# Kernel optimization log

Hardware: AMD Instinct MI355X
Metric: run time of the kernel (lower is better)

Reference implementation:

```python
import jax, jax.numpy as jnp
import numpy as np

N, E, H, L = 20000, 1_280_000, 64, 4


def setup_inputs() -> dict:
    key = jax.random.key(0)
    ks = jax.random.split(key, 24)
    inputs = jax.random.normal(ks[0], (1, N, 6), jnp.float32)
    node_masks = jnp.ones((1, N), jnp.int32)
    send_edges = jax.random.randint(ks[1], (E,), 0, N)
    recv_edges = jax.random.randint(ks[2], (E,), 0, N)

    def w(k, shape, scale=None):
        s = (1.0 / np.sqrt(shape[-2])) if scale is None else scale
        return (jax.random.normal(k, shape, jnp.float32) * s)

    d = dict(
        inputs=inputs, node_masks=node_masks,
        send_edges=send_edges, recv_edges=recv_edges,
        emb_w=w(ks[3], (1, H)), emb_b=jnp.zeros((H,), jnp.float32),
        edge_w1=w(ks[4], (L, 2 * H + 1, H)), edge_b1=jnp.zeros((L, H), jnp.float32),
        edge_w2=w(ks[5], (L, H, H)), edge_b2=jnp.zeros((L, H), jnp.float32),
        node_w1=w(ks[6], (L, 2 * H, H)), node_b1=jnp.zeros((L, H), jnp.float32),
        node_w2=w(ks[7], (L, H, H)), node_b2=jnp.zeros((L, H), jnp.float32),
        coord_w1=w(ks[8], (L, H, H)), coord_b1=jnp.zeros((L, H), jnp.float32),
        coord_wout=w(ks[9], (L, H, 1), scale=0.001),  # xavier gain=0.001, no bias
        vel_w1=w(ks[10], (L, H, H)), vel_b1=jnp.zeros((L, H), jnp.float32),
        vel_w2=w(ks[11], (L, H, 1)), vel_b2=jnp.zeros((L, 1), jnp.float32),
    )
    return d


def reference(inputs, node_masks, send_edges, recv_edges,
              emb_w, emb_b, edge_w1, edge_b1, edge_w2, edge_b2,
              node_w1, node_b1, node_w2, node_b2,
              coord_w1, coord_b1, coord_wout,
              vel_w1, vel_b1, vel_w2, vel_b2):
    silu = jax.nn.silu
    # node_masks is all-ones -> node_inds = arange(N); all nodes active.
    pos, vel = jnp.split(inputs, 2, axis=-1)          # [1,N,3] each
    h = jnp.linalg.norm(vel, axis=-1, keepdims=True)  # speed -> [1,N,1]
    h = h @ emb_w + emb_b                             # [1,N,H]
    coord = pos
    n = coord.shape[1]
    counts = jax.ops.segment_sum(jnp.ones_like(recv_edges, dtype=coord.dtype),
                                 recv_edges, num_segments=n)
    inv_cnt = (1.0 / jnp.maximum(counts, 1.0))[None, :, None]
    seg = lambda e: jax.ops.segment_sum(e, recv_edges, num_segments=n)

    for l in range(L):
        # coord2radial
        cd = coord[:, send_edges] - coord[:, recv_edges]        # [1,E,3]
        radial = jnp.sum(cd * cd, -1, keepdims=True)            # [1,E,1]
        # edge_model
        ef_in = jnp.concatenate([h[:, send_edges], h[:, recv_edges], radial], -1)
        ef = silu(silu(ef_in @ edge_w1[l] + edge_b1[l]) @ edge_w2[l] + edge_b2[l])
        # coord_model
        cm = silu(ef @ coord_w1[l] + coord_b1[l]) @ coord_wout[l]  # [1,E,1]
        trans = jnp.clip(cd * cm, -100.0, 100.0)
        agg_mean = jax.vmap(seg)(trans) * inv_cnt                  # scatter_mean
        # velocity update
        v_gate = silu(h @ vel_w1[l] + vel_b1[l]) @ vel_w2[l] + vel_b2[l]
        vel = agg_mean + v_gate * vel
        coord = coord + vel
        # node_model (recurrent residual)
        agg_sum = jax.vmap(seg)(ef)                                # scatter_sum
        hn = jnp.concatenate([h, agg_sum], -1)
        h = silu(hn @ node_w1[l] + node_b1[l]) @ node_w2[l] + node_b2[l] + h

    pred = jnp.concatenate([coord, vel], -1)  # [1,N,6] == pred_all (all active)
    return pred
```

## Files before the change

### kernel.cpp

```cpp
#include <hip/hip_runtime.h>
#include <math.h>

#define N_NODES 20000
#define N_EDGES 1280000
#define NLAYERS 4
#define NTILE (N_EDGES/32)
#define TSTRIDE 68

typedef short bf16x8 __attribute__((ext_vector_type(8)));
typedef float f32x4  __attribute__((ext_vector_type(4)));
typedef long long i64;
typedef unsigned short us;

__device__ __forceinline__ float silu_f(float x) {
    return x / (1.0f + __expf(-x));
}

__device__ __forceinline__ us f2b(float x) {
    union { float f; unsigned u; } v; v.f = x;
    unsigned r = v.u + 0x7FFF + ((v.u >> 16) & 1);
    return (us)(r >> 16);
}
__device__ __forceinline__ float b2f(us u) {
    union { float f; unsigned u; } v; v.u = ((unsigned)u) << 16;
    return v.f;
}
__device__ __forceinline__ void split2r(float x, us& hi, us& lo) {
    hi = f2b(x);
    lo = f2b(x - b2f(hi));
}
__device__ __forceinline__ void split2f(float x, us& hi, us& lo) {
    union { float f; unsigned u; } v; v.f = x;
    hi = (us)(v.u >> 16);
    union { float f; unsigned u; } h; h.u = v.u & 0xFFFF0000u;
    union { float f; unsigned u; } r; r.f = x - h.f;
    lo = (us)(r.u >> 16);
}

__device__ __forceinline__ bf16x8 ld8(const us* p) {
    bf16x8 a;
    ((i64*)&a)[0] = *(const i64*)p;
    ((i64*)&a)[1] = *(const i64*)(p + 4);
    return a;
}

__device__ __forceinline__ void mfma3(f32x4& acc, bf16x8 ahi, bf16x8 alo,
                                      bf16x8 bhi, bf16x8 blo) {
    acc = __builtin_amdgcn_mfma_f32_16x16x32_bf16(ahi, bhi, acc, 0, 0, 0);
    acc = __builtin_amdgcn_mfma_f32_16x16x32_bf16(alo, bhi, acc, 0, 0, 0);
    acc = __builtin_amdgcn_mfma_f32_16x16x32_bf16(ahi, blo, acc, 0, 0, 0);
}

__global__ void k_init(const float* __restrict__ inp,
                       const float* __restrict__ emb_w,
                       const float* __restrict__ emb_b,
                       float* __restrict__ outv,
                       us* __restrict__ hbh, us* __restrict__ hbl) {
    int t = blockIdx.x * blockDim.x + threadIdx.x;
    int n = t >> 6, f = t & 63;
    if (n >= N_NODES) return;
    float vx = inp[n*6+3], vy = inp[n*6+4], vz = inp[n*6+5];
    float sp = sqrtf(vx*vx + vy*vy + vz*vz);
    float hv = sp * emb_w[f] + emb_b[f];
    us hi, lo; split2r(hv, hi, lo);
    hbh[t] = hi; hbl[t] = lo;
    if (f < 6) outv[n*6+f] = inp[n*6+f];
}

__global__ void k_cnt(const int* __restrict__ recv, int* __restrict__ counts) {
    int t = blockIdx.x*256 + threadIdx.x;
    if (t < N_EDGES) atomicAdd(&counts[recv[t]], 1);
}

__global__ void k_scan(const int* __restrict__ counts, int* __restrict__ rowstart,
                       int* __restrict__ cursor) {
    __shared__ int buf[256];
    __shared__ int carry;
    const int tid = threadIdx.x;
    if (tid == 0) carry = 0;
    __syncthreads();
    for (int base = 0; base < N_NODES; base += 256) {
        const int i = base + tid;
        int v = (i < N_NODES) ? counts[i] : 0;
        buf[tid] = v;
        __syncthreads();
        for (int off = 1; off < 256; off <<= 1) {
            int tv = (tid >= off) ? buf[tid-off] : 0;
            __syncthreads();
            buf[tid] += tv;
            __syncthreads();
        }
        const int excl = buf[tid] - v;
        if (i < N_NODES) { int rv = carry + excl; rowstart[i] = rv; cursor[i] = rv; }
        __syncthreads();
        if (tid == 255) carry += buf[255];
        __syncthreads();
    }
    if (tid < 20) rowstart[N_NODES + tid] = N_EDGES;
}

__global__ void k_scatter(const int* __restrict__ send, const int* __restrict__ recv,
                          int* __restrict__ cursor, us* __restrict__ sp16) {
    int t = blockIdx.x*256 + threadIdx.x;
    if (t < N_EDGES) {
        int p = atomicAdd(&cursor[recv[t]], 1);
        sp16[p] = (us)send[t];
    }
}

__global__ void k_tilemap(const int* __restrict__ rowstart, int* __restrict__ tile2node) {
    int b = blockIdx.x*256 + threadIdx.x;
    if (b >= NTILE) return;
    const int e = b*32;
    int lo = 0, hi = N_NODES-1;
    while (lo < hi) {
        int mid = (lo+hi+1) >> 1;
        if (rowstart[mid] <= e) lo = mid; else hi = mid-1;
    }
    tile2node[b] = lo;
}

__global__ void k_prepw(const float* __restrict__ ew1, const float* __restrict__ ew2,
                        const float* __restrict__ cw1,
                        us* __restrict__ w1th, us* __restrict__ w1tl,
                        us* __restrict__ w2th, us* __restrict__ w2tl,
                        us* __restrict__ cw1th, us* __restrict__ cw1tl) {
    int t = blockIdx.x*256 + threadIdx.x;
    int l = t >> 14;
    int r = t & 16383;
    us hi, lo;
    if (r < 8192) {
        int n = r >> 7, k = r & 127;
        split2r(ew1[l*129*64 + k*64 + n], hi, lo);
        w1th[l*8192 + r] = hi; w1tl[l*8192 + r] = lo;
    } else if (r < 12288) {
        int rr = r - 8192; int n = rr >> 6, k = rr & 63;
        split2r(ew2[l*4096 + k*64 + n], hi, lo);
        w2th[l*4096 + n*64 + k] = hi; w2tl[l*4096 + n*64 + k] = lo;
    } else {
        int rr = r - 12288; int n = rr >> 6, k = rr & 63;
        split2r(cw1[l*4096 + k*64 + n], hi, lo);
        cw1th[l*4096 + n*64 + k] = hi; cw1tl[l*4096 + n*64 + k] = lo;
    }
}

__launch_bounds__(256, 4)
__global__ void k_edge(const us* __restrict__ sp16, const int* __restrict__ rowstart,
                       const int* __restrict__ tile2node,
                       const us* __restrict__ hbh, const us* __restrict__ hbl,
                       const float* __restrict__ outv,
                       const us* __restrict__ w1th, const us* __restrict__ w1tl,
                       const us* __restrict__ w2th, const us* __restrict__ w2tl,
                       const us* __restrict__ cw1th, const us* __restrict__ cw1tl,
                       const float* __restrict__ ew1, const float* __restrict__ eb1,
                       const float* __restrict__ eb2, const float* __restrict__ cb1,
                       const float* __restrict__ cwo,
                       float* __restrict__ aggs, float* __restrict__ aggm) {
    __shared__ us tileh[4][32*TSTRIDE];
    __shared__ us tilel[4][32*TSTRIDE];

    const int tid  = threadIdx.x;
    const int wid  = tid >> 6;
    const int lane = tid & 63;
    const int q    = lane >> 4;
    const int l15  = lane & 15;
    const int wbase = blockIdx.x*128 + wid*32;
    const int wtile = blockIdx.x*4 + wid;

    const int e0 = wbase + l15, e1 = e0 + 16;
    const int s0 = sp16[e0], s1 = sp16[e1];

    const int t2n = tile2node[wtile];
    const int wv = rowstart[t2n + 1 + l15];
    int seg0 = 0, seg1 = 0;
    #pragma unroll
    for (int i = 0; i < 16; ++i) {
        const int wi = __shfl(wv, i);
        seg0 += (e0 >= wi);
        seg1 += (e1 >= wi);
    }
    const int r0 = t2n + seg0, r1 = t2n + seg1;

    const float cdx0 = outv[s0*6+0]-outv[r0*6+0], cdy0 = outv[s0*6+1]-outv[r0*6+1], cdz0 = outv[s0*6+2]-outv[r0*6+2];
    const float cdx1 = outv[s1*6+0]-outv[r1*6+0], cdy1 = outv[s1*6+1]-outv[r1*6+1], cdz1 = outv[s1*6+2]-outv[r1*6+2];
    const float rad0 = cdx0*cdx0+cdy0*cdy0+cdz0*cdz0;
    const float rad1 = cdx1*cdx1+cdy1*cdy1+cdz1*cdz1;

    f32x4 acc[2][4];
    #pragma unroll
    for (int mu = 0; mu < 2; ++mu)
        #pragma unroll
        for (int t = 0; t < 4; ++t) acc[mu][t] = (f32x4){0.f,0.f,0.f,0.f};

    #pragma unroll
    for (int kc = 0; kc < 4; ++kc) {
        const int off = (kc & 1)*32 + q*8;
        const size_t o0 = (size_t)((kc < 2) ? s0 : r0)*64 + off;
        const size_t o1 = (size_t)((kc < 2) ? s1 : r1)*64 + off;
        bf16x8 a0h = ld8(hbh + o0), a0l = ld8(hbl + o0);
        bf16x8 a1h = ld8(hbh + o1), a1l = ld8(hbl + o1);
        #pragma unroll
        for (int t = 0; t < 4; ++t) {
            const int wo = (16*t + l15)*128 + kc*32 + q*8;
            bf16x8 bh = ld8(w1th + wo), bl = ld8(w1tl + wo);
            mfma3(acc[0][t], a0h, a0l, bh, bl);
            mfma3(acc[1][t], a1h, a1l, bh, bl);
        }
    }

    float rsh0[4], rsh1[4];
    #pragma unroll
    for (int r = 0; r < 4; ++r) {
        rsh0[r] = __shfl(rad0, 4*q + r);
        rsh1[r] = __shfl(rad1, 4*q + r);
    }
    #pragma unroll
    for (int t = 0; t < 4; ++t) {
        const int col = 16*t + l15;
        const float wl = ew1[128*64 + col];
        const float bb = eb1[col];
        #pragma unroll
        for (int r = 0; r < 4; ++r) {
            acc[0][t][r] += rsh0[r]*wl + bb;
            acc[1][t][r] += rsh1[r]*wl + bb;
        }
    }

    us* Th = tileh[wid];
    us* Tl = tilel[wid];
    #pragma unroll
    for (int mu = 0; mu < 2; ++mu)
        #pragma unroll
        for (int t = 0; t < 4; ++t)
            #pragma unroll
            for (int r = 0; r < 4; ++r) {
                us hi, lo; split2f(silu_f(acc[mu][t][r]), hi, lo);
                const int ti = (mu*16 + 4*q + r)*TSTRIDE + 16*t + l15;
                Th[ti] = hi; Tl[ti] = lo;
            }
    __asm__ volatile("s_waitcnt lgkmcnt(0)" ::: "memory");

    #pragma unroll
    for (int mu = 0; mu < 2; ++mu)
        #pragma unroll
        for (int t = 0; t < 4; ++t) acc[mu][t] = (f32x4){0.f,0.f,0.f,0.f};
    #pragma unroll
    for (int kc = 0; kc < 2; ++kc) {
        const int t0 = l15*TSTRIDE + kc*32 + q*8;
        const int t1i = (16+l15)*TSTRIDE + kc*32 + q*8;
        bf16x8 a0h = ld8(Th + t0),  a0l = ld8(Tl + t0);
        bf16x8 a1h = ld8(Th + t1i), a1l = ld8(Tl + t1i);
        #pragma unroll
        for (int t = 0; t < 4; ++t) {
            const int wo = (16*t + l15)*64 + kc*32 + q*8;
            bf16x8 bh = ld8(w2th + wo), bl = ld8(w2tl + wo);
            mfma3(acc[0][t], a0h, a0l, bh, bl);
            mfma3(acc[1][t], a1h, a1l, bh, bl);
        }
    }

    float ef[2][4][4];
    #pragma unroll
    for (int t = 0; t < 4; ++t) {
        const float bb = eb2[16*t + l15];
        #pragma unroll
        for (int mu = 0; mu < 2; ++mu)
            #pragma unroll
            for (int r = 0; r < 4; ++r)
                ef[mu][t][r] = silu_f(acc[mu][t][r] + bb);
    }
    __asm__ volatile("s_waitcnt lgkmcnt(0)" ::: "memory");
    #pragma unroll
    for (int mu = 0; mu < 2; ++mu)
        #pragma unroll
        for (int t = 0; t < 4; ++t)
            #pragma unroll
            for (int r = 0; r < 4; ++r) {
                us hi, lo; split2f(ef[mu][t][r], hi, lo);
                const int ti = (mu*16 + 4*q + r)*TSTRIDE + 16*t + l15;
                Th[ti] = hi; Tl[ti] = lo;
            }
    __asm__ volatile("s_waitcnt lgkmcnt(0)" ::: "memory");

    #pragma unroll
    for (int mu = 0; mu < 2; ++mu)
        #pragma unroll
        for (int t = 0; t < 4; ++t) acc[mu][t] = (f32x4){0.f,0.f,0.f,0.f};
    #pragma unroll
    for (int kc = 0; kc < 2; ++kc) {
        const int t0 = l15*TSTRIDE + kc*32 + q*8;
        const int t1i = (16+l15)*TSTRIDE + kc*32 + q*8;
        bf16x8 a0h = ld8(Th + t0),  a0l = ld8(Tl + t0);
        bf16x8 a1h = ld8(Th + t1i), a1l = ld8(Tl + t1i);
        #pragma unroll
        for (int t = 0; t < 4; ++t) {
            const int wo = (16*t + l15)*64 + kc*32 + q*8;
            bf16x8 bh = ld8(cw1th + wo), bl = ld8(cw1tl + wo);
            mfma3(acc[0][t], a0h, a0l, bh, bl);
            mfma3(acc[1][t], a1h, a1l, bh, bl);
        }
    }

    float cm0[4] = {0.f,0.f,0.f,0.f}, cm1[4] = {0.f,0.f,0.f,0.f};
    #pragma unroll
    for (int t = 0; t < 4; ++t) {
        const int col = 16*t + l15;
        const float cb = cb1[col];
        const float co = cwo[col];
        #pragma unroll
        for (int r = 0; r < 4; ++r) {
            cm0[r] += silu_f(acc[0][t][r] + cb) * co;
            cm1[r] += silu_f(acc[1][t][r] + cb) * co;
        }
    }
    #pragma unroll
    for (int m = 1; m <= 8; m <<= 1)
        #pragma unroll
        for (int r = 0; r < 4; ++r) {
            cm0[r] += __shfl_xor(cm0[r], m);
            cm1[r] += __shfl_xor(cm1[r], m);
        }

    int   sgrow[2][4];
    float tv[2][4];
    #pragma unroll
    for (int mu = 0; mu < 2; ++mu)
        #pragma unroll
        for (int r = 0; r < 4; ++r) {
            sgrow[mu][r] = __shfl(mu ? seg1 : seg0, 4*q + r);
            const float cxv = __shfl(mu ? cdx1 : cdx0, 4*q + r);
            const float cyv = __shfl(mu ? cdy1 : cdy0, 4*q + r);
            const float czv = __shfl(mu ? cdz1 : cdz0, 4*q + r);
            const float cmv = mu ? cm1[r] : cm0[r];
            const float sel = (l15 == 0) ? cxv : (l15 == 1) ? cyv : czv;
            tv[mu][r] = (l15 < 3) ? fminf(fmaxf(sel*cmv, -100.f), 100.f) : 0.f;
        }

    const int segA = __shfl(seg0, 0);
    const int segB = __shfl(seg1, 15);

    if (segB == segA) {
        float s4[4], trT = 0.f;
        #pragma unroll
        for (int t = 0; t < 4; ++t) {
            float v = 0.f;
            #pragma unroll
            for (int mu = 0; mu < 2; ++mu)
                #pragma unroll
                for (int r = 0; r < 4; ++r) v += ef[mu][t][r];
            v += __shfl_xor(v, 16);
            v += __shfl_xor(v, 32);
            s4[t] = v;
        }
        #pragma unroll
        for (int mu = 0; mu < 2; ++mu)
            #pragma unroll
            for (int r = 0; r < 4; ++r) trT += tv[mu][r];
        trT += __shfl_xor(trT, 16);
        trT += __shfl_xor(trT, 32);
        const int rn = t2n + segA;
        if (q == 0) {
            #pragma unroll
            for (int t = 0; t < 4; ++t)
                atomicAdd(&aggs[(size_t)rn*64 + 16*t + l15], s4[t]);
            if (l15 < 3) atomicAdd(&aggm[rn*3 + l15], trT);
        }
    } else if (segB == segA + 1) {
        float sA[4] = {0,0,0,0}, sB[4] = {0,0,0,0};
        float trA = 0.f, trB = 0.f;
        #pragma unroll
        for (int mu = 0; mu < 2; ++mu)
            #pragma unroll
            for (int r = 0; r < 4; ++r) {
                const bool isA = (sgrow[mu][r] == segA);
                #pragma unroll
                for (int t = 0; t < 4; ++t) {
                    const float v = ef[mu][t][r];
                    sA[t] += isA ? v : 0.f;
                    sB[t] += isA ? 0.f : v;
                }
                const float tvv = tv[mu][r];
                trA += isA ? tvv : 0.f;
                trB += isA ? 0.f : tvv;
            }
        #pragma unroll
        for (int t = 0; t < 4; ++t) {
            sA[t] += __shfl_xor(sA[t], 16); sA[t] += __shfl_xor(sA[t], 32);
            sB[t] += __shfl_xor(sB[t], 16); sB[t] += __shfl_xor(sB[t], 32);
        }
        trA += __shfl_xor(trA, 16); trA += __shfl_xor(trA, 32);
        trB += __shfl_xor(trB, 16); trB += __shfl_xor(trB, 32);
        const int rnA = t2n + segA, rnB = rnA + 1;
        if (q == 0) {
            #pragma unroll
            for (int t = 0; t < 4; ++t) {
                atomicAdd(&aggs[(size_t)rnA*64 + 16*t + l15], sA[t]);
                atomicAdd(&aggs[(size_t)rnB*64 + 16*t + l15], sB[t]);
            }
            if (l15 < 3) {
                atomicAdd(&aggm[rnA*3 + l15], trA);
                atomicAdd(&aggm[rnB*3 + l15], trB);
            }
        }
    } else {
        #pragma unroll
        for (int mu = 0; mu < 2; ++mu)
            #pragma unroll
            for (int r = 0; r < 4; ++r) {
                const int ren = t2n + sgrow[mu][r];
                #pragma unroll
                for (int t = 0; t < 4; ++t)
                    atomicAdd(&aggs[(size_t)ren*64 + 16*t + l15], ef[mu][t][r]);
                if (l15 < 3) atomicAdd(&aggm[ren*3 + l15], tv[mu][r]);
            }
    }
}

__launch_bounds__(256, 4)
__global__ void k_node(const float* __restrict__ aggs, const float* __restrict__ aggm,
                       const int* __restrict__ rowstart,
                       const float* __restrict__ VW1, const float* __restrict__ vb1,
                       const float* __restrict__ VW2, const float* __restrict__ vb2,
                       const float* __restrict__ NW1, const float* __restrict__ nb1,
                       const float* __restrict__ NW2, const float* __restrict__ nb2,
                       float* __restrict__ outv,
                       us* __restrict__ hbh, us* __restrict__ hbl) {
    __shared__ float hs[4][64], as[4][64], tt[4][64];
    const int tid = threadIdx.x;
    const int nn = tid >> 6, f = tid & 63;
    const int n = blockIdx.x*4 + nn;
    float hv = b2f(hbh[n*64+f]) + b2f(hbl[n*64+f]);
    hs[nn][f] = hv;
    as[nn][f] = aggs[n*64+f];
    __syncthreads();

    float a1 = vb1[f];
    for (int k = 0; k < 64; ++k) a1 += hs[nn][k] * VW1[k*64+f];
    float p = silu_f(a1) * VW2[f];
    #pragma unroll
    for (int o = 32; o > 0; o >>= 1) p += __shfl_down(p, o);
    float vgate = __shfl(p, 0) + vb2[0];

    if (f < 3) {
        float icnt = 1.0f / fmaxf((float)(rowstart[n+1] - rowstart[n]), 1.0f);
        float nv = aggm[n*3+f]*icnt + vgate*outv[n*6+3+f];
        outv[n*6+3+f] = nv;
        outv[n*6+f]  += nv;
    }

    float b = nb1[f];
    for (int k = 0; k < 64; ++k) b += hs[nn][k]*NW1[k*64+f];
    for (int k = 0; k < 64; ++k) b += as[nn][k]*NW1[(64+k)*64+f];
    __syncthreads();
    tt[nn][f] = silu_f(b);
    __syncthreads();
    float o = nb2[f] + hv;
    for (int k = 0; k < 64; ++k) o += tt[nn][k]*NW2[k*64+f];
    us hi, lo; split2r(o, hi, lo);
    hbh[n*64+f] = hi; hbl[n*64+f] = lo;
}

extern "C" void kernel_launch(void* const* d_in, const int* in_sizes, int n_in,
                              void* d_out, int out_size, void* d_ws, size_t ws_size,
                              hipStream_t stream) {
    const float* inp   = (const float*)d_in[0];
    const int*   send  = (const int*)d_in[2];
    const int*   recv  = (const int*)d_in[3];
    const float* emb_w = (const float*)d_in[4];
    const float* emb_b = (const float*)d_in[5];
    const float* ew1   = (const float*)d_in[6];
    const float* eb1   = (const float*)d_in[7];
    const float* ew2   = (const float*)d_in[8];
    const float* eb2   = (const float*)d_in[9];
    const float* nw1   = (const float*)d_in[10];
    const float* nb1   = (const float*)d_in[11];
    const float* nw2   = (const float*)d_in[12];
    const float* nb2   = (const float*)d_in[13];
    const float* cw1   = (const float*)d_in[14];
    const float* cb1   = (const float*)d_in[15];
    const float* cwo   = (const float*)d_in[16];
    const float* vw1   = (const float*)d_in[17];
    const float* vb1   = (const float*)d_in[18];
    const float* vw2   = (const float*)d_in[19];
    const float* vb2   = (const float*)d_in[20];

    float* outv = (float*)d_out;

    float* ws        = (float*)d_ws;
    float* aggs      = ws;
    float* aggm      = aggs + (size_t)N_NODES*64;
    int*   rowstart  = (int*)(aggm + N_NODES*3);
    int*   tile2node = rowstart + (N_NODES+20);
    us*    hbh       = (us*)(tile2node + NTILE);
    us*    hbl       = hbh + (size_t)N_NODES*64;
    us*    sp16      = hbl + (size_t)N_NODES*64;
    us*    w1th      = sp16 + N_EDGES;
    us*    w1tl      = w1th + 4*8192;
    us*    w2th      = w1tl + 4*8192;
    us*    w2tl      = w2th + 4*4096;
    us*    cw1th     = w2tl + 4*4096;
    us*    cw1tl     = cw1th + 4*4096;
    int*   counts    = (int*)aggs;
    int*   cursor    = counts + N_NODES;

    hipMemsetAsync(counts, 0, N_NODES*sizeof(int), stream);
    k_init<<<(N_NODES*64)/256, 256, 0, stream>>>(inp, emb_w, emb_b, outv, hbh, hbl);
    k_cnt<<<(N_EDGES+255)/256, 256, 0, stream>>>(recv, counts);
    k_scan<<<1, 256, 0, stream>>>(counts, rowstart, cursor);
    k_scatter<<<(N_EDGES+255)/256, 256, 0, stream>>>(send, recv, cursor, sp16);
    k_tilemap<<<(NTILE+255)/256, 256, 0, stream>>>(rowstart, tile2node);
    k_prepw<<<256, 256, 0, stream>>>(ew1, ew2, cw1, w1th, w1tl, w2th, w2tl, cw1th, cw1tl);

    for (int l = 0; l < NLAYERS; ++l) {
        hipMemsetAsync(aggs, 0, (size_t)N_NODES*67*sizeof(float), stream);
        k_edge<<<N_EDGES/128, 256, 0, stream>>>(sp16, rowstart, tile2node, hbh, hbl, outv,
            w1th + l*8192, w1tl + l*8192,
            w2th + l*4096, w2tl + l*4096,
            cw1th + l*4096, cw1tl + l*4096,
            ew1 + (size_t)l*129*64, eb1 + l*64, eb2 + l*64,
            cb1 + l*64, cwo + l*64,
            aggs, aggm);
        k_node<<<N_NODES/4, 256, 0, stream>>>(aggs, aggm, rowstart,
            vw1 + (size_t)l*64*64, vb1 + l*64, vw2 + l*64, vb2 + l,
            nw1 + (size_t)l*128*64, nb1 + l*64,
            nw2 + (size_t)l*64*64,  nb2 + l*64,
            outv, hbh, hbl);
    }
}
```

Baseline: 2.082 ms.

## Process edge halves sequentially for occupancy, fuse tilemap into scan, drop memsets

The edge kernel now runs its three-GEMM MLP chain on each 16-edge half in turn instead of both halves together. This halves the LDS tile and accumulator registers, so launch bounds rise from 4 to 6 waves per SIMD. The tile-to-node map is built inside a chunked single-block scan, removing the binary-search kernel. The per-layer memset of the aggregation buffers is replaced by zeroing them in the node kernel after they are read. The cost is less instruction-level parallelism per wave and a more serial scan.

```diff
diff --git a/kernel.cpp b/kernel.cpp
--- a/kernel.cpp
+++ b/kernel.cpp
@@ -6,6 +6,7 @@
 #define NLAYERS 4
 #define NTILE (N_EDGES/32)
 #define TSTRIDE 68
+#define SCHUNK 79
 
 typedef short bf16x8 __attribute__((ext_vector_type(8)));
 typedef float f32x4  __attribute__((ext_vector_type(4)));
@@ -73,28 +74,27 @@
 }
 
 __global__ void k_scan(const int* __restrict__ counts, int* __restrict__ rowstart,
-                       int* __restrict__ cursor) {
+                       int* __restrict__ cursor, int* __restrict__ tile2node) {
     __shared__ int buf[256];
-    __shared__ int carry;
     const int tid = threadIdx.x;
-    if (tid == 0) carry = 0;
+    const int lo = tid*SCHUNK;
+    const int hi = (lo + SCHUNK < N_NODES) ? lo + SCHUNK : N_NODES;
+    int s = 0;
+    for (int i = lo; i < hi; ++i) s += counts[i];
+    buf[tid] = s;
     __syncthreads();
-    for (int base = 0; base < N_NODES; base += 256) {
-        const int i = base + tid;
-        int v = (i < N_NODES) ? counts[i] : 0;
-        buf[tid] = v;
+    for (int off = 1; off < 256; off <<= 1) {
+        int v = (tid >= off) ? buf[tid-off] : 0;
         __syncthreads();
-        for (int off = 1; off < 256; off <<= 1) {
-            int tv = (tid >= off) ? buf[tid-off] : 0;
-            __syncthreads();
-            buf[tid] += tv;
-            __syncthreads();
-        }
-        const int excl = buf[tid] - v;
-        if (i < N_NODES) { int rv = carry + excl; rowstart[i] = rv; cursor[i] = rv; }
+        buf[tid] += v;
         __syncthreads();
-        if (tid == 255) carry += buf[255];
-        __syncthreads();
+    }
+    int run = buf[tid] - s;
+    for (int i = lo; i < hi; ++i) {
+        rowstart[i] = run; cursor[i] = run;
+        const int c = counts[i];
+        for (int t = (run + 31) >> 5; t*32 < run + c; ++t) tile2node[t] = i;
+        run += c;
     }
     if (tid < 20) rowstart[N_NODES + tid] = N_EDGES;
 }
@@ -106,18 +106,6 @@
         int p = atomicAdd(&cursor[recv[t]], 1);
         sp16[p] = (us)send[t];
     }
-}
-
-__global__ void k_tilemap(const int* __restrict__ rowstart, int* __restrict__ tile2node) {
-    int b = blockIdx.x*256 + threadIdx.x;
-    if (b >= NTILE) return;
-    const int e = b*32;
-    int lo = 0, hi = N_NODES-1;
-    while (lo < hi) {
-        int mid = (lo+hi+1) >> 1;
-        if (rowstart[mid] <= e) lo = mid; else hi = mid-1;
-    }
-    tile2node[b] = lo;
 }
 
 __global__ void k_prepw(const float* __restrict__ ew1, const float* __restrict__ ew2,
@@ -144,7 +132,7 @@
     }
 }
 
-__launch_bounds__(256, 4)
+__launch_bounds__(256, 6)
 __global__ void k_edge(const us* __restrict__ sp16, const int* __restrict__ rowstart,
                        const int* __restrict__ tile2node,
                        const us* __restrict__ hbh, const us* __restrict__ hbl,
@@ -156,8 +144,8 @@
                        const float* __restrict__ eb2, const float* __restrict__ cb1,
                        const float* __restrict__ cwo,
                        float* __restrict__ aggs, float* __restrict__ aggm) {
-    __shared__ us tileh[4][32*TSTRIDE];
-    __shared__ us tilel[4][32*TSTRIDE];
+    __shared__ us tileh[4][16*TSTRIDE];
+    __shared__ us tilel[4][16*TSTRIDE];
 
     const int tid  = threadIdx.x;
     const int wid  = tid >> 6;
@@ -186,140 +174,126 @@
     const float rad0 = cdx0*cdx0+cdy0*cdy0+cdz0*cdz0;
     const float rad1 = cdx1*cdx1+cdy1*cdy1+cdz1*cdz1;
 
-    f32x4 acc[2][4];
-    #pragma unroll
-    for (int mu = 0; mu < 2; ++mu)
-        #pragma unroll
-        for (int t = 0; t < 4; ++t) acc[mu][t] = (f32x4){0.f,0.f,0.f,0.f};
-
-    #pragma unroll
-    for (int kc = 0; kc < 4; ++kc) {
-        const int off = (kc & 1)*32 + q*8;
-        const size_t o0 = (size_t)((kc < 2) ? s0 : r0)*64 + off;
-        const size_t o1 = (size_t)((kc < 2) ? s1 : r1)*64 + off;
-        bf16x8 a0h = ld8(hbh + o0), a0l = ld8(hbl + o0);
-        bf16x8 a1h = ld8(hbh + o1), a1l = ld8(hbl + o1);
-        #pragma unroll
-        for (int t = 0; t < 4; ++t) {
-            const int wo = (16*t + l15)*128 + kc*32 + q*8;
-            bf16x8 bh = ld8(w1th + wo), bl = ld8(w1tl + wo);
-            mfma3(acc[0][t], a0h, a0l, bh, bl);
-            mfma3(acc[1][t], a1h, a1l, bh, bl);
-        }
-    }
-
-    float rsh0[4], rsh1[4];
-    #pragma unroll
-    for (int r = 0; r < 4; ++r) {
-        rsh0[r] = __shfl(rad0, 4*q + r);
-        rsh1[r] = __shfl(rad1, 4*q + r);
-    }
+    float wlv[4], b1v[4], eb2v[4], cb1v[4], cwov[4];
     #pragma unroll
     for (int t = 0; t < 4; ++t) {
         const int col = 16*t + l15;
-        const float wl = ew1[128*64 + col];
-        const float bb = eb1[col];
-        #pragma unroll
-        for (int r = 0; r < 4; ++r) {
-            acc[0][t][r] += rsh0[r]*wl + bb;
-            acc[1][t][r] += rsh1[r]*wl + bb;
-        }
+        wlv[t]  = ew1[128*64 + col];
+        b1v[t]  = eb1[col];
+        eb2v[t] = eb2[col];
+        cb1v[t] = cb1[col];
+        cwov[t] = cwo[col];
     }
 
     us* Th = tileh[wid];
     us* Tl = tilel[wid];
+
+    float ef[2][4][4];
+    float cm[2][4];
+
     #pragma unroll
-    for (int mu = 0; mu < 2; ++mu)
+    for (int mu = 0; mu < 2; ++mu) {
+        const int   sE   = mu ? s1 : s0;
+        const int   rE   = mu ? r1 : r0;
+        const float radE = mu ? rad1 : rad0;
+
+        f32x4 acc[4];
+        #pragma unroll
+        for (int t = 0; t < 4; ++t) acc[t] = (f32x4){0.f,0.f,0.f,0.f};
+        #pragma unroll
+        for (int kc = 0; kc < 4; ++kc) {
+            const int off = (kc & 1)*32 + q*8;
+            const size_t oA = (size_t)((kc < 2) ? sE : rE)*64 + off;
+            bf16x8 ah = ld8(hbh + oA), al = ld8(hbl + oA);
+            #pragma unroll
+            for (int t = 0; t < 4; ++t) {
+                const int wo = (16*t + l15)*128 + kc*32 + q*8;
+                bf16x8 bh = ld8(w1th + wo), bl = ld8(w1tl + wo);
+                mfma3(acc[t], ah, al, bh, bl);
+            }
+        }
+
+        float rsh[4];
+        #pragma unroll
+        for (int r = 0; r < 4; ++r) rsh[r] = __shfl(radE, 4*q + r);
         #pragma unroll
         for (int t = 0; t < 4; ++t)
             #pragma unroll
+            for (int r = 0; r < 4; ++r)
+                acc[t][r] += rsh[r]*wlv[t] + b1v[t];
+
+        #pragma unroll
+        for (int t = 0; t < 4; ++t)
+            #pragma unroll
             for (int r = 0; r < 4; ++r) {
-                us hi, lo; split2f(silu_f(acc[mu][t][r]), hi, lo);
-                const int ti = (mu*16 + 4*q + r)*TSTRIDE + 16*t + l15;
+                us hi, lo; split2f(silu_f(acc[t][r]), hi, lo);
+                const int ti = (4*q + r)*TSTRIDE + 16*t + l15;
                 Th[ti] = hi; Tl[ti] = lo;
             }
-    __asm__ volatile("s_waitcnt lgkmcnt(0)" ::: "memory");
-
-    #pragma unroll
-    for (int mu = 0; mu < 2; ++mu)
-        #pragma unroll
-        for (int t = 0; t < 4; ++t) acc[mu][t] = (f32x4){0.f,0.f,0.f,0.f};
-    #pragma unroll
-    for (int kc = 0; kc < 2; ++kc) {
-        const int t0 = l15*TSTRIDE + kc*32 + q*8;
-        const int t1i = (16+l15)*TSTRIDE + kc*32 + q*8;
-        bf16x8 a0h = ld8(Th + t0),  a0l = ld8(Tl + t0);
-        bf16x8 a1h = ld8(Th + t1i), a1l = ld8(Tl + t1i);
-        #pragma unroll
-        for (int t = 0; t < 4; ++t) {
-            const int wo = (16*t + l15)*64 + kc*32 + q*8;
-            bf16x8 bh = ld8(w2th + wo), bl = ld8(w2tl + wo);
-            mfma3(acc[0][t], a0h, a0l, bh, bl);
-            mfma3(acc[1][t], a1h, a1l, bh, bl);
-        }
-    }
-
-    float ef[2][4][4];
-    #pragma unroll
-    for (int t = 0; t < 4; ++t) {
-        const float bb = eb2[16*t + l15];
-        #pragma unroll
-        for (int mu = 0; mu < 2; ++mu)
+        __asm__ volatile("s_waitcnt lgkmcnt(0)" ::: "memory");
+
+        f32x4 acc2[4];
+        #pragma unroll
+        for (int t = 0; t < 4; ++t) acc2[t] = (f32x4){0.f,0.f,0.f,0.f};
+        #pragma unroll
+        for (int kc = 0; kc < 2; ++kc) {
+            const int to = l15*TSTRIDE + kc*32 + q*8;
+            bf16x8 ah = ld8(Th + to), al = ld8(Tl + to);
+            #pragma unroll
+            for (int t = 0; t < 4; ++t) {
+                const int wo = (16*t + l15)*64 + kc*32 + q*8;
+                bf16x8 bh = ld8(w2th + wo), bl = ld8(w2tl + wo);
+                mfma3(acc2[t], ah, al, bh, bl);
+            }
+        }
+
+        #pragma unroll
+        for (int t = 0; t < 4; ++t)
             #pragma unroll
             for (int r = 0; r < 4; ++r)
-                ef[mu][t][r] = silu_f(acc[mu][t][r] + bb);
-    }
-    __asm__ volatile("s_waitcnt lgkmcnt(0)" ::: "memory");
-    #pragma unroll
-    for (int mu = 0; mu < 2; ++mu)
+                ef[mu][t][r] = silu_f(acc2[t][r] + eb2v[t]);
+        __asm__ volatile("s_waitcnt lgkmcnt(0)" ::: "memory");
         #pragma unroll
         for (int t = 0; t < 4; ++t)
             #pragma unroll
             for (int r = 0; r < 4; ++r) {
                 us hi, lo; split2f(ef[mu][t][r], hi, lo);
-                const int ti = (mu*16 + 4*q + r)*TSTRIDE + 16*t + l15;
+                const int ti = (4*q + r)*TSTRIDE + 16*t + l15;
                 Th[ti] = hi; Tl[ti] = lo;
             }
-    __asm__ volatile("s_waitcnt lgkmcnt(0)" ::: "memory");
-
-    #pragma unroll
-    for (int mu = 0; mu < 2; ++mu)
-        #pragma unroll
-        for (int t = 0; t < 4; ++t) acc[mu][t] = (f32x4){0.f,0.f,0.f,0.f};
-    #pragma unroll
-    for (int kc = 0; kc < 2; ++kc) {
-        const int t0 = l15*TSTRIDE + kc*32 + q*8;
-        const int t1i = (16+l15)*TSTRIDE + kc*32 + q*8;
-        bf16x8 a0h = ld8(Th + t0),  a0l = ld8(Tl + t0);
-        bf16x8 a1h = ld8(Th + t1i), a1l = ld8(Tl + t1i);
-        #pragma unroll
-        for (int t = 0; t < 4; ++t) {
-            const int wo = (16*t + l15)*64 + kc*32 + q*8;
-            bf16x8 bh = ld8(cw1th + wo), bl = ld8(cw1tl + wo);
-            mfma3(acc[0][t], a0h, a0l, bh, bl);
-            mfma3(acc[1][t], a1h, a1l, bh, bl);
-        }
-    }
-
-    float cm0[4] = {0.f,0.f,0.f,0.f}, cm1[4] = {0.f,0.f,0.f,0.f};
-    #pragma unroll
-    for (int t = 0; t < 4; ++t) {
-        const int col = 16*t + l15;
-        const float cb = cb1[col];
-        const float co = cwo[col];
-        #pragma unroll
-        for (int r = 0; r < 4; ++r) {
-            cm0[r] += silu_f(acc[0][t][r] + cb) * co;
-            cm1[r] += silu_f(acc[1][t][r] + cb) * co;
-        }
-    }
-    #pragma unroll
-    for (int m = 1; m <= 8; m <<= 1)
-        #pragma unroll
-        for (int r = 0; r < 4; ++r) {
-            cm0[r] += __shfl_xor(cm0[r], m);
-            cm1[r] += __shfl_xor(cm1[r], m);
-        }
+        __asm__ volatile("s_waitcnt lgkmcnt(0)" ::: "memory");
+
+        f32x4 acc3[4];
+        #pragma unroll
+        for (int t = 0; t < 4; ++t) acc3[t] = (f32x4){0.f,0.f,0.f,0.f};
+        #pragma unroll
+        for (int kc = 0; kc < 2; ++kc) {
+            const int to = l15*TSTRIDE + kc*32 + q*8;
+            bf16x8 ah = ld8(Th + to), al = ld8(Tl + to);
+            #pragma unroll
+            for (int t = 0; t < 4; ++t) {
+                const int wo = (16*t + l15)*64 + kc*32 + q*8;
+                bf16x8 bh = ld8(cw1th + wo), bl = ld8(cw1tl + wo);
+                mfma3(acc3[t], ah, al, bh, bl);
+            }
+        }
+
+        float cmE[4] = {0.f,0.f,0.f,0.f};
+        #pragma unroll
+        for (int t = 0; t < 4; ++t)
+            #pragma unroll
+            for (int r = 0; r < 4; ++r)
+                cmE[r] += silu_f(acc3[t][r] + cb1v[t]) * cwov[t];
+        #pragma unroll
+        for (int m = 1; m <= 8; m <<= 1)
+            #pragma unroll
+            for (int r = 0; r < 4; ++r)
+                cmE[r] += __shfl_xor(cmE[r], m);
+        #pragma unroll
+        for (int r = 0; r < 4; ++r) cm[mu][r] = cmE[r];
+
+        __asm__ volatile("s_waitcnt lgkmcnt(0)" ::: "memory");
+    }
 
     int   sgrow[2][4];
     float tv[2][4];
@@ -331,7 +305,7 @@
             const float cxv = __shfl(mu ? cdx1 : cdx0, 4*q + r);
             const float cyv = __shfl(mu ? cdy1 : cdy0, 4*q + r);
             const float czv = __shfl(mu ? cdz1 : cdz0, 4*q + r);
-            const float cmv = mu ? cm1[r] : cm0[r];
+            const float cmv = cm[mu][r];
             const float sel = (l15 == 0) ? cxv : (l15 == 1) ? cyv : czv;
             tv[mu][r] = (l15 < 3) ? fminf(fmaxf(sel*cmv, -100.f), 100.f) : 0.f;
         }
@@ -417,7 +391,7 @@
 }
 
 __launch_bounds__(256, 4)
-__global__ void k_node(const float* __restrict__ aggs, const float* __restrict__ aggm,
+__global__ void k_node(float* __restrict__ aggs, float* __restrict__ aggm,
                        const int* __restrict__ rowstart,
                        const float* __restrict__ VW1, const float* __restrict__ vb1,
                        const float* __restrict__ VW2, const float* __restrict__ vb2,
@@ -432,6 +406,7 @@
     float hv = b2f(hbh[n*64+f]) + b2f(hbl[n*64+f]);
     hs[nn][f] = hv;
     as[nn][f] = aggs[n*64+f];
+    aggs[n*64+f] = 0.f;
     __syncthreads();
 
     float a1 = vb1[f];
@@ -444,6 +419,7 @@
     if (f < 3) {
         float icnt = 1.0f / fmaxf((float)(rowstart[n+1] - rowstart[n]), 1.0f);
         float nv = aggm[n*3+f]*icnt + vgate*outv[n*6+3+f];
+        aggm[n*3+f] = 0.f;
         outv[n*6+3+f] = nv;
         outv[n*6+f]  += nv;
     }
@@ -506,13 +482,12 @@
     hipMemsetAsync(counts, 0, N_NODES*sizeof(int), stream);
     k_init<<<(N_NODES*64)/256, 256, 0, stream>>>(inp, emb_w, emb_b, outv, hbh, hbl);
     k_cnt<<<(N_EDGES+255)/256, 256, 0, stream>>>(recv, counts);
-    k_scan<<<1, 256, 0, stream>>>(counts, rowstart, cursor);
+    k_scan<<<1, 256, 0, stream>>>(counts, rowstart, cursor, tile2node);
     k_scatter<<<(N_EDGES+255)/256, 256, 0, stream>>>(send, recv, cursor, sp16);
-    k_tilemap<<<(NTILE+255)/256, 256, 0, stream>>>(rowstart, tile2node);
     k_prepw<<<256, 256, 0, stream>>>(ew1, ew2, cw1, w1th, w1tl, w2th, w2tl, cw1th, cw1tl);
+    hipMemsetAsync(aggs, 0, (size_t)N_NODES*67*sizeof(float), stream);
 
     for (int l = 0; l < NLAYERS; ++l) {
-        hipMemsetAsync(aggs, 0, (size_t)N_NODES*67*sizeof(float), stream);
         k_edge<<<N_EDGES/128, 256, 0, stream>>>(sp16, rowstart, tile2node, hbh, hbl, outv,
             w1th + l*8192, w1tl + l*8192,
             w2th + l*4096, w2tl + l*4096,
```

Result: slower. 3.214 ms (+54.4%).
